# Kernel optimization log

Measured on AMD Instinct MI355X. Metric: run time of the kernel, lower is better.

## Reference

```python
import jax, jax.numpy as jnp
import numpy as np

N, C, E, K = 50000, 128, 640000, 40  # nodes, feat dim, edges, classes
EPS = 1e-5


def setup_inputs() -> dict:
    key = jax.random.key(0)
    ks = jax.random.split(key, 8)
    s = 1.0 / np.sqrt(C)
    return {
        "x": jax.random.normal(ks[0], (N, C), jnp.float32),
        "edge_index": jax.random.randint(ks[1], (2, E), 0, N, dtype=jnp.int32),
        "W_conv": jax.random.normal(ks[2], (C, C), jnp.float32) * s,
        "b_conv": jnp.zeros((C,), jnp.float32),
        "gamma": jnp.ones((C,), jnp.float32),
        "beta": jnp.zeros((C,), jnp.float32),
        "W_fc": jax.random.normal(ks[3], (C, K), jnp.float32) * s,
        "b_fc": jnp.zeros((K,), jnp.float32),
    }


def reference(x, edge_index, W_conv, b_conv, gamma, beta, W_fc, b_fc):
    n = x.shape[0]
    loops = jnp.arange(n, dtype=edge_index.dtype)
    src = jnp.concatenate([edge_index[0], loops])  # add self-loops (PyG default)
    dst = jnp.concatenate([edge_index[1], loops])
    # symmetric normalization: deg^{-1/2}[src] * deg^{-1/2}[dst]
    deg = jax.ops.segment_sum(jnp.ones_like(dst, jnp.float32), dst, num_segments=n)
    dinv = jax.lax.rsqrt(jnp.maximum(deg, 1.0))  # deg >= 1 with self-loops
    norm = dinv[src] * dinv[dst]  # [E+N]
    h = x @ W_conv  # [N, C] transform before propagate (GCNConv)
    agg = jax.ops.segment_sum(h[src] * norm[:, None], dst, num_segments=n) + b_conv
    a = jax.nn.relu(agg) * x  # dropout = identity (eval mode); elementwise mul with residual
    mu = jnp.mean(a, axis=-1, keepdims=True)
    var = jnp.mean((a - mu) ** 2, axis=-1, keepdims=True)
    ln = (a - mu) * jax.lax.rsqrt(var + EPS) * gamma + beta
    return (ln + x) @ W_fc + b_fc
```

## Files before the change

### kernel.cpp

```cpp
#include <hip/hip_runtime.h>

#define C_DIM 128
#define EPS 1e-5f
#define NBIN 784
#define SBLK 2048

typedef __attribute__((ext_vector_type(8))) short short8;
typedef __attribute__((ext_vector_type(4))) float f32x4;

__device__ __forceinline__ unsigned bf16rn(float f) {
    unsigned u = __float_as_uint(f);
    return (u + 0x7fffu + ((u >> 16) & 1u)) >> 16;
}
__device__ __forceinline__ unsigned pack_bf16(float lo, float hi) {
    return bf16rn(lo) | (bf16rn(hi) << 16);
}
__device__ __forceinline__ float blo(unsigned u) { return __uint_as_float(u << 16); }
__device__ __forceinline__ float bhi(unsigned u) { return __uint_as_float(u & 0xffff0000u); }

__device__ __forceinline__ void wave_scan_excl_lds(unsigned* buf, int lane) {
    const int CH = (NBIN + 63) / 64;
    unsigned v[CH];
    unsigned s = 0;
    int c0 = lane * CH;
#pragma unroll
    for (int k = 0; k < CH; k++) {
        int idx = c0 + k;
        v[k] = (idx < NBIN) ? buf[idx] : 0u;
        s += v[k];
    }
    unsigned inc = s;
#pragma unroll
    for (int off = 1; off < 64; off <<= 1) {
        unsigned tmp = __shfl_up(inc, off);
        if (lane >= off) inc += tmp;
    }
    unsigned run = inc - s;
#pragma unroll
    for (int k = 0; k < CH; k++) {
        int idx = c0 + k;
        if (idx < NBIN) { buf[idx] = run; run += v[k]; }
    }
}

__global__ __launch_bounds__(256) void k_hist(const float* __restrict__ W,
                                              const float* __restrict__ Wfc,
                                              unsigned short* __restrict__ WhT,
                                              unsigned short* __restrict__ WlT,
                                              unsigned short* __restrict__ WT,
                                              const int* __restrict__ edst,
                                              unsigned* __restrict__ H, int e, int ns) {
    __shared__ unsigned lh[NBIN];
    int b = blockIdx.x, t = threadIdx.x;
    if (b < ns) {
        for (int k = t; k < NBIN; k += 256) lh[k] = 0u;
        __syncthreads();
        int e0 = b * SBLK;
        int lim = e - e0; if (lim > SBLK) lim = SBLK;
        for (int k = t; k < lim; k += 256) atomicAdd(&lh[edst[e0 + k] >> 6], 1u);
        __syncthreads();
        for (int k = t; k < NBIN; k += 256) H[(size_t)b * NBIN + k] = lh[k];
    } else {
        int gid = (b - ns) * 256 + t;
        int stride = ((int)gridDim.x - ns) * 256;
        for (int i = gid; i < 128 * 128; i += stride) {
            int c = i >> 7, k = i & 127;
            float v = W[k * 128 + c];
            unsigned hi = bf16rn(v);
            WhT[c * 128 + k] = (unsigned short)hi;
            WlT[c * 128 + k] = (unsigned short)bf16rn(v - __uint_as_float(hi << 16));
        }
        for (int i = gid; i < 48 * 128; i += stride) {
            int nc = i >> 7, k = i & 127;
            WT[nc * 128 + k] = (unsigned short)((nc < 40) ? bf16rn(Wfc[k * 40 + nc]) : 0u);
        }
    }
}

__global__ __launch_bounds__(256) void k_scan(unsigned* __restrict__ H,
                                              unsigned* __restrict__ tot, int ns) {
    int bin = blockIdx.x * 4 + (threadIdx.x >> 6);
    int lane = threadIdx.x & 63;
    if (bin >= NBIN) return;
    unsigned run = 0;
    for (int base = 0; base < ns; base += 64) {
        int idx = base + lane;
        unsigned v = (idx < ns) ? H[(size_t)idx * NBIN + bin] : 0u;
        unsigned inc = v;
#pragma unroll
        for (int off = 1; off < 64; off <<= 1) {
            unsigned tmp = __shfl_up(inc, off);
            if (lane >= off) inc += tmp;
        }
        if (idx < ns) H[(size_t)idx * NBIN + bin] = run + inc - v;
        run += __shfl(inc, 63);
    }
    if (lane == 0) tot[bin] = run;
}

__global__ void k_binscan(const unsigned* __restrict__ tot, unsigned* __restrict__ bstart) {
    int lane = threadIdx.x;
    const int CH = (NBIN + 63) / 64;
    unsigned v[CH];
    unsigned s = 0;
    int c0 = lane * CH;
#pragma unroll
    for (int k = 0; k < CH; k++) {
        int idx = c0 + k;
        v[k] = (idx < NBIN) ? tot[idx] : 0u;
        s += v[k];
    }
    unsigned inc = s;
#pragma unroll
    for (int off = 1; off < 64; off <<= 1) {
        unsigned tmp = __shfl_up(inc, off);
        if (lane >= off) inc += tmp;
    }
    unsigned run = inc - s;
#pragma unroll
    for (int k = 0; k < CH; k++) {
        int idx = c0 + k;
        if (idx < NBIN) { bstart[idx] = run; run += v[k]; }
    }
    if (lane == 63) bstart[NBIN] = run;
}

__global__ __launch_bounds__(256, 4) void k_sort(const float* __restrict__ x,
                                                 const unsigned short* __restrict__ WhT,
                                                 const unsigned short* __restrict__ WlT,
                                                 unsigned short* __restrict__ hbs,
                                                 const int* __restrict__ esrc,
                                                 const int* __restrict__ edst,
                                                 const unsigned* __restrict__ H,
                                                 const unsigned* __restrict__ bstart,
                                                 unsigned* __restrict__ recs,
                                                 int n, int e, int ns) {
    __shared__ unsigned bufA[NBIN];
    __shared__ unsigned bufB[NBIN];
    __shared__ unsigned bufC[NBIN];
    __shared__ unsigned sbuf[SBLK];
    int b = blockIdx.x, t = threadIdx.x;

    if (b < ns) {
        int e0 = b * SBLK;
        int myE = e - e0; if (myE > SBLK) myE = SBLK;
        for (int k = t; k < NBIN; k += 256) { bufC[k] = 0u; bufA[k] = 0u; }
        __syncthreads();
        for (int k = t; k < myE; k += 256) atomicAdd(&bufC[edst[e0 + k] >> 6], 1u);
        for (int bin = t; bin < NBIN; bin += 256)
            bufB[bin] = bstart[bin] + H[(size_t)b * NBIN + bin];
        __syncthreads();
        if (t < 64) wave_scan_excl_lds(bufC, t);
        __syncthreads();
        for (int k = t; k < myE; k += 256) {
            int d = edst[e0 + k];
            int s = esrc[e0 + k];
            int bin = d >> 6;
            unsigned lr = atomicAdd(&bufA[bin], 1u);
            sbuf[bufC[bin] + lr] =
                ((unsigned)bin << 22) | ((unsigned)(d & 63) << 16) | (unsigned)s;
        }
        __syncthreads();
        for (int j = t; j < myE; j += 256) {
            unsigned rec = sbuf[j];
            unsigned bin = rec >> 22;
            recs[bufB[bin] + (unsigned)j - bufC[bin]] = rec;
        }
    } else {
        int r0 = (b - ns) * 128;
        int wid = t >> 6, lane = t & 63;
        int mrow = lane & 15, quad = lane >> 4;
        int rb = r0 + wid * 32;

        f32x4 acc[2][8];
#pragma unroll
        for (int m = 0; m < 2; m++)
#pragma unroll
            for (int nn = 0; nn < 8; nn++) acc[m][nn] = (f32x4){0.f, 0.f, 0.f, 0.f};

#pragma unroll
        for (int ks = 0; ks < 4; ks++) {
            short8 Ah[2], Al[2];
#pragma unroll
            for (int m = 0; m < 2; m++) {
                int r = rb + m * 16 + mrow;
                if (r >= n) r = n - 1;
                const float* xp = &x[(long)r * C_DIM + ks * 32 + quad * 8];
                float4 va = *(const float4*)xp;
                float4 vb = *(const float4*)(xp + 4);
                float xv[8] = {va.x, va.y, va.z, va.w, vb.x, vb.y, vb.z, vb.w};
#pragma unroll
                for (int e8 = 0; e8 < 8; e8++) {
                    unsigned hi = bf16rn(xv[e8]);
                    Ah[m][e8] = (short)hi;
                    Al[m][e8] = (short)bf16rn(xv[e8] - __uint_as_float(hi << 16));
                }
            }
#pragma unroll
            for (int nn = 0; nn < 8; nn++) {
                int wof = (nn * 16 + mrow) * 128 + ks * 32 + quad * 8;
                short8 Bh = *(const short8*)&WhT[wof];
                short8 Bl = *(const short8*)&WlT[wof];
#pragma unroll
                for (int m = 0; m < 2; m++) {
                    acc[m][nn] = __builtin_amdgcn_mfma_f32_16x16x32_bf16(Ah[m], Bh, acc[m][nn], 0, 0, 0);
                    acc[m][nn] = __builtin_amdgcn_mfma_f32_16x16x32_bf16(Al[m], Bh, acc[m][nn], 0, 0, 0);
                    acc[m][nn] = __builtin_amdgcn_mfma_f32_16x16x32_bf16(Ah[m], Bl, acc[m][nn], 0, 0, 0);
                }
            }
        }
#pragma unroll
        for (int m = 0; m < 2; m++)
#pragma unroll
            for (int nn = 0; nn < 8; nn++) {
                int c = nn * 16 + mrow;
#pragma unroll
                for (int reg = 0; reg < 4; reg++) {
                    int r = rb + m * 16 + quad * 4 + reg;
                    if (r < n) hbs[(long)r * 128 + c] = (unsigned short)bf16rn(acc[m][nn][reg]);
                }
            }
    }
}

__global__ __launch_bounds__(256) void k_csr(const unsigned* __restrict__ recs,
                                             const unsigned* __restrict__ bstart,
                                             const unsigned* __restrict__ hb,
                                             unsigned* __restrict__ hb2,
                                             unsigned short* __restrict__ csr,
                                             unsigned* __restrict__ rowptr, int n) {
    __shared__ unsigned nh[64], nstart[64], cur[64];
    __shared__ float dinvl[64];
    __shared__ unsigned short sl[4096];
    int bin = blockIdx.x, t = threadIdx.x;
    unsigned s0 = bstart[bin];
    unsigned cn = bstart[bin + 1] - s0;
    if (t < 64) { nh[t] = 0u; cur[t] = 0u; }
    __syncthreads();
    for (unsigned k = t; k < cn; k += 256) atomicAdd(&nh[(recs[s0 + k] >> 16) & 63u], 1u);
    __syncthreads();
    if (t < 64) {
        unsigned v = nh[t];
        unsigned inc = v;
#pragma unroll
        for (int off = 1; off < 64; off <<= 1) {
            unsigned tmp = __shfl_up(inc, off);
            if (t >= off) inc += tmp;
        }
        unsigned excl = inc - v;
        nstart[t] = excl;
        rowptr[bin * 64 + t] = s0 + excl;
        dinvl[t] = rsqrtf((float)v + 1.0f);
    }
    __syncthreads();
    for (unsigned k = t; k < cn; k += 256) {
        unsigned rec = recs[s0 + k];
        unsigned nd = (rec >> 16) & 63u;
        unsigned r = atomicAdd(&cur[nd], 1u);
        unsigned idx = nstart[nd] + r;
        if (idx < 4096) sl[idx] = (unsigned short)(rec & 0xFFFFu);
        else csr[s0 + idx] = (unsigned short)(rec & 0xFFFFu);
    }
    __syncthreads();
    for (unsigned k = t; k < cn && k < 4096; k += 256) csr[s0 + k] = sl[k];
    for (int idx = t; idx < 1024; idx += 256) {
        int row = idx >> 4;
        int node = bin * 64 + row;
        if (node < n) {
            float di = dinvl[row];
            uint4 u = ((const uint4*)hb)[(size_t)node * 16 + (idx & 15)];
            uint4 o;
            o.x = pack_bf16(di * blo(u.x), di * bhi(u.x));
            o.y = pack_bf16(di * blo(u.y), di * bhi(u.y));
            o.z = pack_bf16(di * blo(u.z), di * bhi(u.z));
            o.w = pack_bf16(di * blo(u.w), di * bhi(u.w));
            ((uint4*)hb2)[(size_t)node * 16 + (idx & 15)] = o;
        }
    }
}

__global__ __launch_bounds__(256) void aggregate(const unsigned* __restrict__ hb2,
                                                 const float* __restrict__ x,
                                                 const unsigned short* __restrict__ csr,
                                                 const unsigned* __restrict__ rowptr,
                                                 const float* __restrict__ bconv,
                                                 const float* __restrict__ gamma,
                                                 const float* __restrict__ beta,
                                                 unsigned* __restrict__ zb, int n) {
    int wid = (blockIdx.x * blockDim.x + threadIdx.x) >> 6;
    if (wid >= n) return;
    int lane = threadIdx.x & 63;
    int sub = lane & 15, grp = lane >> 4;
    int i = wid;

    unsigned rs = rowptr[i];
    unsigned re = rowptr[i + 1];
    int deg = (int)(re - rs);
    float di = rsqrtf((float)deg + 1.0f);

    uint4 us = *(const uint4*)(hb2 + (long)i * 64 + sub * 4);
    float4 xa = *(const float4*)&x[(long)i * C_DIM + sub * 8];
    float4 xb = *(const float4*)&x[(long)i * C_DIM + sub * 8 + 4];
    int s_all = (int)csr[rs + lane];

    float wself = (grp == 0) ? 1.f : 0.f;
    float acc[8];
    acc[0] = wself * blo(us.x); acc[1] = wself * bhi(us.x);
    acc[2] = wself * blo(us.y); acc[3] = wself * bhi(us.y);
    acc[4] = wself * blo(us.z); acc[5] = wself * bhi(us.z);
    acc[6] = wself * blo(us.w); acc[7] = wself * bhi(us.w);

    int nIt = (deg + 15) >> 4;
    for (int it = 0; it < nIt; ++it) {
        int ss[4];
        float ww[4];
#pragma unroll
        for (int qq = 0; qq < 4; qq++) {
            int base = it * 16 + qq * 4;
            int tq = base + grp;
            int sq;
            if (base >= 64) sq = (int)csr[rs + tq];
            else sq = __shfl(s_all, tq);
            float wq = 1.f;
            if (tq >= deg) { wq = 0.f; sq = i; }
            ss[qq] = sq;
            ww[qq] = wq;
        }
        uint4 u[4];
#pragma unroll
        for (int qq = 0; qq < 4; qq++) u[qq] = *(const uint4*)(hb2 + (long)ss[qq] * 64 + sub * 4);
#pragma unroll
        for (int qq = 0; qq < 4; qq++) {
            float w = ww[qq];
            acc[0] += w * blo(u[qq].x); acc[1] += w * bhi(u[qq].x);
            acc[2] += w * blo(u[qq].y); acc[3] += w * bhi(u[qq].y);
            acc[4] += w * blo(u[qq].z); acc[5] += w * bhi(u[qq].z);
            acc[6] += w * blo(u[qq].w); acc[7] += w * bhi(u[qq].w);
        }
    }

#pragma unroll
    for (int j = 0; j < 8; j++) {
        acc[j] += __shfl_xor(acc[j], 16);
        acc[j] += __shfl_xor(acc[j], 32);
    }

    float4 bca = *(const float4*)&bconv[sub * 8];
    float4 bcb = *(const float4*)&bconv[sub * 8 + 4];
    float a[8], xv[8];
    xv[0] = xa.x; xv[1] = xa.y; xv[2] = xa.z; xv[3] = xa.w;
    xv[4] = xb.x; xv[5] = xb.y; xv[6] = xb.z; xv[7] = xb.w;
    float bc[8] = {bca.x, bca.y, bca.z, bca.w, bcb.x, bcb.y, bcb.z, bcb.w};
#pragma unroll
    for (int j = 0; j < 8; j++) a[j] = fmaxf(acc[j] * di + bc[j], 0.f) * xv[j];

    float s = a[0] + a[1] + a[2] + a[3] + a[4] + a[5] + a[6] + a[7];
#pragma unroll
    for (int off = 1; off < 16; off <<= 1) s += __shfl_xor(s, off);
    float mu = s * (1.0f / 128.0f);
    float d[8], v = 0.f;
#pragma unroll
    for (int j = 0; j < 8; j++) { d[j] = a[j] - mu; v += d[j] * d[j]; }
#pragma unroll
    for (int off = 1; off < 16; off <<= 1) v += __shfl_xor(v, off);
    float inv = rsqrtf(v * (1.0f / 128.0f) + EPS);

    if (grp == 0) {
        float4 ga = *(const float4*)&gamma[sub * 8];
        float4 gb = *(const float4*)&gamma[sub * 8 + 4];
        float4 ba = *(const float4*)&beta[sub * 8];
        float4 bb = *(const float4*)&beta[sub * 8 + 4];
        float g[8] = {ga.x, ga.y, ga.z, ga.w, gb.x, gb.y, gb.z, gb.w};
        float be[8] = {ba.x, ba.y, ba.z, ba.w, bb.x, bb.y, bb.z, bb.w};
        float o[8];
#pragma unroll
        for (int j = 0; j < 8; j++) o[j] = d[j] * inv * g[j] + be[j] + xv[j];
        uint4 p;
        p.x = pack_bf16(o[0], o[1]);
        p.y = pack_bf16(o[2], o[3]);
        p.z = pack_bf16(o[4], o[5]);
        p.w = pack_bf16(o[6], o[7]);
        *(uint4*)(zb + (long)i * 64 + sub * 4) = p;
    }
}

__global__ __launch_bounds__(256) void gemm2(const unsigned short* __restrict__ zb,
                                             const unsigned short* __restrict__ WT,
                                             const float* __restrict__ bfc,
                                             float* __restrict__ out, int n) {
    int t = threadIdx.x;
    int w = t >> 6, lane = t & 63;
    int r0 = blockIdx.x * 64 + w * 16;
    if (r0 >= n) return;
    int mrow = lane & 15;
    int quad = lane >> 4;
    f32x4 acc[3];
#pragma unroll
    for (int nt = 0; nt < 3; nt++) acc[nt] = (f32x4){0.f, 0.f, 0.f, 0.f};
#pragma unroll
    for (int ks = 0; ks < 4; ks++) {
        int r = r0 + mrow;
        if (r >= n) r = n - 1;
        short8 A = *(const short8*)&zb[(long)r * 128 + ks * 32 + quad * 8];
        short8 B[3];
#pragma unroll
        for (int nt = 0; nt < 3; nt++)
            B[nt] = *(const short8*)&WT[(nt * 16 + mrow) * 128 + ks * 32 + quad * 8];
#pragma unroll
        for (int nt = 0; nt < 3; nt++)
            acc[nt] = __builtin_amdgcn_mfma_f32_16x16x32_bf16(A, B[nt], acc[nt], 0, 0, 0);
    }
#pragma unroll
    for (int nt = 0; nt < 3; nt++) {
        int c = nt * 16 + mrow;
        if (c < 40) {
            float bias = bfc[c];
#pragma unroll
            for (int reg = 0; reg < 4; reg++) {
                int r = r0 + quad * 4 + reg;
                if (r < n) out[(long)r * 40 + c] = acc[nt][reg] + bias;
            }
        }
    }
}

extern "C" void kernel_launch(void* const* d_in, const int* in_sizes, int n_in,
                              void* d_out, int out_size, void* d_ws, size_t ws_size,
                              hipStream_t stream) {
    const float* x     = (const float*)d_in[0];
    const int*   ei    = (const int*)d_in[1];
    const float* Wc    = (const float*)d_in[2];
    const float* bc    = (const float*)d_in[3];
    const float* gamma = (const float*)d_in[4];
    const float* beta  = (const float*)d_in[5];
    const float* Wfc   = (const float*)d_in[6];
    const float* bfc   = (const float*)d_in[7];
    float* out = (float*)d_out;

    int N = in_sizes[0] / C_DIM;
    int E = in_sizes[1] / 2;
    const int* esrc = ei;
    const int* edst = ei + E;
    int ns = (E + SBLK - 1) / SBLK;
    int g1 = (N + 127) / 128;

    char* p = (char*)d_ws;
    auto carve = [&](size_t bytes) {
        void* q = (void*)p;
        p += (bytes + 255) & ~(size_t)255;
        return q;
    };
    unsigned* hb         = (unsigned*)carve((size_t)N * 64 * 4);
    unsigned* hb2        = (unsigned*)carve((size_t)N * 64 * 4);
    unsigned short* WT   = (unsigned short*)carve(48 * 128 * 2);
    unsigned short* WhT  = (unsigned short*)carve(128 * 128 * 2);
    unsigned short* WlT  = (unsigned short*)carve(128 * 128 * 2);
    unsigned* H          = (unsigned*)carve((size_t)ns * NBIN * 4);
    unsigned* tot        = (unsigned*)carve((size_t)NBIN * 4);
    unsigned* bstart     = (unsigned*)carve((size_t)(NBIN + 1) * 4);
    unsigned* recs       = (unsigned*)carve((size_t)E * 4);
    unsigned* rowptr     = (unsigned*)carve((size_t)(NBIN * 64 + 1) * 4);
    unsigned short* csr  = (unsigned short*)carve((size_t)E * 2 + 256);

    unsigned* zb = hb;

    k_hist<<<ns + 64, 256, 0, stream>>>(Wc, Wfc, WhT, WlT, WT, edst, H, E, ns);
    k_scan<<<NBIN / 4, 256, 0, stream>>>(H, tot, ns);
    k_binscan<<<1, 64, 0, stream>>>(tot, bstart);
    k_sort<<<ns + g1, 256, 0, stream>>>(x, WhT, WlT, (unsigned short*)hb, esrc, edst,
                                        H, bstart, recs, N, E, ns);
    k_csr<<<NBIN, 256, 0, stream>>>(recs, bstart, hb, hb2, csr, rowptr, N);
    aggregate<<<((size_t)N * 64 + 255) / 256, 256, 0, stream>>>(
        hb2, x, csr, rowptr, bc, gamma, beta, zb, N);
    gemm2<<<(N + 63) / 64, 256, 0, stream>>>((const unsigned short*)zb, WT, bfc, out, N);
}
```

Measured before the change: 171.7 us.

## Fuse output GEMM into aggregation and fold bin scan into sort kernel

The per-node aggregation kernel now runs 16 nodes per 1024-thread block, stages the bf16 LayerNorm output in LDS, and has three waves do the final 128x40 MFMA GEMM directly. This removes the zb global round trip and the separate gemm2 launch. Separately, the single-wave k_binscan launch is removed: every sort block recomputes the exclusive scan of bin totals in LDS, and block 0 writes bstart for later kernels. The cost is redundant scan work per block, plus a block-wide sync in the aggregate kernel with most waves idle during the GEMM.

After: 174.5 us. About the same (+1.6%).

```diff
diff --git a/kernel.cpp b/kernel.cpp
--- a/kernel.cpp
+++ b/kernel.cpp
@@ -18,7 +18,8 @@
 __device__ __forceinline__ float blo(unsigned u) { return __uint_as_float(u << 16); }
 __device__ __forceinline__ float bhi(unsigned u) { return __uint_as_float(u & 0xffff0000u); }
 
-__device__ __forceinline__ void wave_scan_excl_lds(unsigned* buf, int lane) {
+__device__ __forceinline__ void wave_scan_excl_lds(unsigned* buf, int lane,
+                                                   unsigned* dumpb) {
     const int CH = (NBIN + 63) / 64;
     unsigned v[CH];
     unsigned s = 0;
@@ -39,8 +40,13 @@
 #pragma unroll
     for (int k = 0; k < CH; k++) {
         int idx = c0 + k;
-        if (idx < NBIN) { buf[idx] = run; run += v[k]; }
-    }
+        if (idx < NBIN) {
+            if (dumpb) dumpb[idx] = run;
+            buf[idx] = run;
+            run += v[k];
+        }
+    }
+    if (dumpb && lane == 63) dumpb[NBIN] = run;
 }
 
 __global__ __launch_bounds__(256) void k_hist(const float* __restrict__ W,
@@ -98,33 +104,6 @@
     if (lane == 0) tot[bin] = run;
 }
 
-__global__ void k_binscan(const unsigned* __restrict__ tot, unsigned* __restrict__ bstart) {
-    int lane = threadIdx.x;
-    const int CH = (NBIN + 63) / 64;
-    unsigned v[CH];
-    unsigned s = 0;
-    int c0 = lane * CH;
-#pragma unroll
-    for (int k = 0; k < CH; k++) {
-        int idx = c0 + k;
-        v[k] = (idx < NBIN) ? tot[idx] : 0u;
-        s += v[k];
-    }
-    unsigned inc = s;
-#pragma unroll
-    for (int off = 1; off < 64; off <<= 1) {
-        unsigned tmp = __shfl_up(inc, off);
-        if (lane >= off) inc += tmp;
-    }
-    unsigned run = inc - s;
-#pragma unroll
-    for (int k = 0; k < CH; k++) {
-        int idx = c0 + k;
-        if (idx < NBIN) { bstart[idx] = run; run += v[k]; }
-    }
-    if (lane == 63) bstart[NBIN] = run;
-}
-
 __global__ __launch_bounds__(256, 4) void k_sort(const float* __restrict__ x,
                                                  const unsigned short* __restrict__ WhT,
                                                  const unsigned short* __restrict__ WlT,
@@ -132,7 +111,8 @@
                                                  const int* __restrict__ esrc,
                                                  const int* __restrict__ edst,
                                                  const unsigned* __restrict__ H,
-                                                 const unsigned* __restrict__ bstart,
+                                                 const unsigned* __restrict__ tot,
+                                                 unsigned* __restrict__ bstart,
                                                  unsigned* __restrict__ recs,
                                                  int n, int e, int ns) {
     __shared__ unsigned bufA[NBIN];
@@ -147,11 +127,14 @@
         for (int k = t; k < NBIN; k += 256) { bufC[k] = 0u; bufA[k] = 0u; }
         __syncthreads();
         for (int k = t; k < myE; k += 256) atomicAdd(&bufC[edst[e0 + k] >> 6], 1u);
+        for (int bin = t; bin < NBIN; bin += 256) bufB[bin] = tot[bin];
+        __syncthreads();
+        int wv = t >> 6, lane = t & 63;
+        if (wv == 0) wave_scan_excl_lds(bufC, lane, 0);
+        else if (wv == 1) wave_scan_excl_lds(bufB, lane, b == 0 ? bstart : 0);
+        __syncthreads();
         for (int bin = t; bin < NBIN; bin += 256)
-            bufB[bin] = bstart[bin] + H[(size_t)b * NBIN + bin];
-        __syncthreads();
-        if (t < 64) wave_scan_excl_lds(bufC, t);
-        __syncthreads();
+            bufB[bin] += H[(size_t)b * NBIN + bin];
         for (int k = t; k < myE; k += 256) {
             int d = edst[e0 + k];
             int s = esrc[e0 + k];
@@ -279,28 +262,32 @@
     }
 }
 
-__global__ __launch_bounds__(256) void aggregate(const unsigned* __restrict__ hb2,
-                                                 const float* __restrict__ x,
-                                                 const unsigned short* __restrict__ csr,
-                                                 const unsigned* __restrict__ rowptr,
-                                                 const float* __restrict__ bconv,
-                                                 const float* __restrict__ gamma,
-                                                 const float* __restrict__ beta,
-                                                 unsigned* __restrict__ zb, int n) {
-    int wid = (blockIdx.x * blockDim.x + threadIdx.x) >> 6;
-    if (wid >= n) return;
-    int lane = threadIdx.x & 63;
+__global__ __launch_bounds__(1024) void agg2(const unsigned* __restrict__ hb2,
+                                             const float* __restrict__ x,
+                                             const unsigned short* __restrict__ csr,
+                                             const unsigned* __restrict__ rowptr,
+                                             const float* __restrict__ bconv,
+                                             const float* __restrict__ gamma,
+                                             const float* __restrict__ beta,
+                                             const unsigned short* __restrict__ WT,
+                                             const float* __restrict__ bfc,
+                                             float* __restrict__ out, int n) {
+    __shared__ unsigned zl[16 * 65];
+    int t = threadIdx.x;
+    int wv = t >> 6, lane = t & 63;
     int sub = lane & 15, grp = lane >> 4;
-    int i = wid;
-
-    unsigned rs = rowptr[i];
-    unsigned re = rowptr[i + 1];
+    int i = blockIdx.x * 16 + wv;
+    bool vn = i < n;
+    int ii = vn ? i : n - 1;
+
+    unsigned rs = rowptr[ii];
+    unsigned re = rowptr[ii + 1];
     int deg = (int)(re - rs);
     float di = rsqrtf((float)deg + 1.0f);
 
-    uint4 us = *(const uint4*)(hb2 + (long)i * 64 + sub * 4);
-    float4 xa = *(const float4*)&x[(long)i * C_DIM + sub * 8];
-    float4 xb = *(const float4*)&x[(long)i * C_DIM + sub * 8 + 4];
+    uint4 us = *(const uint4*)(hb2 + (long)ii * 64 + sub * 4);
+    float4 xa = *(const float4*)&x[(long)ii * C_DIM + sub * 8];
+    float4 xb = *(const float4*)&x[(long)ii * C_DIM + sub * 8 + 4];
     int s_all = (int)csr[rs + lane];
 
     float wself = (grp == 0) ? 1.f : 0.f;
@@ -322,7 +309,7 @@
             if (base >= 64) sq = (int)csr[rs + tq];
             else sq = __shfl(s_all, tq);
             float wq = 1.f;
-            if (tq >= deg) { wq = 0.f; sq = i; }
+            if (tq >= deg) { wq = 0.f; sq = ii; }
             ss[qq] = sq;
             ww[qq] = wq;
         }
@@ -375,50 +362,35 @@
         float o[8];
 #pragma unroll
         for (int j = 0; j < 8; j++) o[j] = d[j] * inv * g[j] + be[j] + xv[j];
-        uint4 p;
-        p.x = pack_bf16(o[0], o[1]);
-        p.y = pack_bf16(o[2], o[3]);
-        p.z = pack_bf16(o[4], o[5]);
-        p.w = pack_bf16(o[6], o[7]);
-        *(uint4*)(zb + (long)i * 64 + sub * 4) = p;
-    }
-}
-
-__global__ __launch_bounds__(256) void gemm2(const unsigned short* __restrict__ zb,
-                                             const unsigned short* __restrict__ WT,
-                                             const float* __restrict__ bfc,
-                                             float* __restrict__ out, int n) {
-    int t = threadIdx.x;
-    int w = t >> 6, lane = t & 63;
-    int r0 = blockIdx.x * 64 + w * 16;
-    if (r0 >= n) return;
-    int mrow = lane & 15;
-    int quad = lane >> 4;
-    f32x4 acc[3];
-#pragma unroll
-    for (int nt = 0; nt < 3; nt++) acc[nt] = (f32x4){0.f, 0.f, 0.f, 0.f};
-#pragma unroll
-    for (int ks = 0; ks < 4; ks++) {
-        int r = r0 + mrow;
-        if (r >= n) r = n - 1;
-        short8 A = *(const short8*)&zb[(long)r * 128 + ks * 32 + quad * 8];
-        short8 B[3];
-#pragma unroll
-        for (int nt = 0; nt < 3; nt++)
-            B[nt] = *(const short8*)&WT[(nt * 16 + mrow) * 128 + ks * 32 + quad * 8];
-#pragma unroll
-        for (int nt = 0; nt < 3; nt++)
-            acc[nt] = __builtin_amdgcn_mfma_f32_16x16x32_bf16(A, B[nt], acc[nt], 0, 0, 0);
-    }
-#pragma unroll
-    for (int nt = 0; nt < 3; nt++) {
+        zl[wv * 65 + sub * 4 + 0] = pack_bf16(o[0], o[1]);
+        zl[wv * 65 + sub * 4 + 1] = pack_bf16(o[2], o[3]);
+        zl[wv * 65 + sub * 4 + 2] = pack_bf16(o[4], o[5]);
+        zl[wv * 65 + sub * 4 + 3] = pack_bf16(o[6], o[7]);
+    }
+    __syncthreads();
+
+    if (wv < 3) {
+        int nt = wv;
+        int mrow = lane & 15, quad = lane >> 4;
+        f32x4 a2 = (f32x4){0.f, 0.f, 0.f, 0.f};
+#pragma unroll
+        for (int ks = 0; ks < 4; ks++) {
+            union { unsigned u[4]; short8 s8; } au;
+            int zi = mrow * 65 + ks * 16 + quad * 4;
+            au.u[0] = zl[zi + 0];
+            au.u[1] = zl[zi + 1];
+            au.u[2] = zl[zi + 2];
+            au.u[3] = zl[zi + 3];
+            short8 B = *(const short8*)&WT[(nt * 16 + mrow) * 128 + ks * 32 + quad * 8];
+            a2 = __builtin_amdgcn_mfma_f32_16x16x32_bf16(au.s8, B, a2, 0, 0, 0);
+        }
         int c = nt * 16 + mrow;
         if (c < 40) {
             float bias = bfc[c];
 #pragma unroll
             for (int reg = 0; reg < 4; reg++) {
-                int r = r0 + quad * 4 + reg;
-                if (r < n) out[(long)r * 40 + c] = acc[nt][reg] + bias;
+                int r = blockIdx.x * 16 + quad * 4 + reg;
+                if (r < n) out[(long)r * 40 + c] = a2[reg] + bias;
             }
         }
     }
@@ -462,15 +434,11 @@
     unsigned* rowptr     = (unsigned*)carve((size_t)(NBIN * 64 + 1) * 4);
     unsigned short* csr  = (unsigned short*)carve((size_t)E * 2 + 256);
 
-    unsigned* zb = hb;
-
     k_hist<<<ns + 64, 256, 0, stream>>>(Wc, Wfc, WhT, WlT, WT, edst, H, E, ns);
     k_scan<<<NBIN / 4, 256, 0, stream>>>(H, tot, ns);
-    k_binscan<<<1, 64, 0, stream>>>(tot, bstart);
     k_sort<<<ns + g1, 256, 0, stream>>>(x, WhT, WlT, (unsigned short*)hb, esrc, edst,
-                                        H, bstart, recs, N, E, ns);
+                                        H, tot, bstart, recs, N, E, ns);
     k_csr<<<NBIN, 256, 0, stream>>>(recs, bstart, hb, hb2, csr, rowptr, N);
-    aggregate<<<((size_t)N * 64 + 255) / 256, 256, 0, stream>>>(
-        hb2, x, csr, rowptr, bc, gamma, beta, zb, N);
-    gemm2<<<(N + 63) / 64, 256, 0, stream>>>((const unsigned short*)zb, WT, bfc, out, N);
-}
+    agg2<<<(N + 15) / 16, 1024, 0, stream>>>(hb2, x, csr, rowptr, bc, gamma, beta,
+                                             WT, bfc, out, N);
+}
```

## Fold bin scan into sort, drop dinv prescale pass, apply per-edge weights in aggregate

Applied to the files above, without the earlier changes.

Removes the single-block k_binscan launch: every sort block now scans the bin totals itself, and block 0 writes bstart. k_csr no longer rescales h by deg^-1/2 into a second bf16 buffer. Instead it writes a dinv array, and aggregate multiplies each gathered neighbor row by dinv[src] (shuffled from the first 64 lanes, or loaded directly beyond that). The edge-chunk size SBLK is doubled, which halves the number of histogram and sort blocks and shrinks the H matrix. The trade is redundant scans in every sort block and an extra dinv gather per edge in aggregate, against one fewer launch and one fewer full pass over h.

New measurement: 168.8 us. Within noise of the previous version (-1.7%).

```diff
diff --git a/kernel.cpp b/kernel.cpp
--- a/kernel.cpp
+++ b/kernel.cpp
@@ -3,7 +3,7 @@
 #define C_DIM 128
 #define EPS 1e-5f
 #define NBIN 784
-#define SBLK 2048
+#define SBLK 4096
 
 typedef __attribute__((ext_vector_type(8))) short short8;
 typedef __attribute__((ext_vector_type(4))) float f32x4;
@@ -18,7 +18,8 @@
 __device__ __forceinline__ float blo(unsigned u) { return __uint_as_float(u << 16); }
 __device__ __forceinline__ float bhi(unsigned u) { return __uint_as_float(u & 0xffff0000u); }
 
-__device__ __forceinline__ void wave_scan_excl_lds(unsigned* buf, int lane) {
+__device__ __forceinline__ void wave_scan_excl_lds(unsigned* buf, int lane,
+                                                   unsigned* dumpb) {
     const int CH = (NBIN + 63) / 64;
     unsigned v[CH];
     unsigned s = 0;
@@ -39,8 +40,13 @@
 #pragma unroll
     for (int k = 0; k < CH; k++) {
         int idx = c0 + k;
-        if (idx < NBIN) { buf[idx] = run; run += v[k]; }
-    }
+        if (idx < NBIN) {
+            if (dumpb) dumpb[idx] = run;
+            buf[idx] = run;
+            run += v[k];
+        }
+    }
+    if (dumpb && lane == 63) dumpb[NBIN] = run;
 }
 
 __global__ __launch_bounds__(256) void k_hist(const float* __restrict__ W,
@@ -98,33 +104,6 @@
     if (lane == 0) tot[bin] = run;
 }
 
-__global__ void k_binscan(const unsigned* __restrict__ tot, unsigned* __restrict__ bstart) {
-    int lane = threadIdx.x;
-    const int CH = (NBIN + 63) / 64;
-    unsigned v[CH];
-    unsigned s = 0;
-    int c0 = lane * CH;
-#pragma unroll
-    for (int k = 0; k < CH; k++) {
-        int idx = c0 + k;
-        v[k] = (idx < NBIN) ? tot[idx] : 0u;
-        s += v[k];
-    }
-    unsigned inc = s;
-#pragma unroll
-    for (int off = 1; off < 64; off <<= 1) {
-        unsigned tmp = __shfl_up(inc, off);
-        if (lane >= off) inc += tmp;
-    }
-    unsigned run = inc - s;
-#pragma unroll
-    for (int k = 0; k < CH; k++) {
-        int idx = c0 + k;
-        if (idx < NBIN) { bstart[idx] = run; run += v[k]; }
-    }
-    if (lane == 63) bstart[NBIN] = run;
-}
-
 __global__ __launch_bounds__(256, 4) void k_sort(const float* __restrict__ x,
                                                  const unsigned short* __restrict__ WhT,
                                                  const unsigned short* __restrict__ WlT,
@@ -132,7 +111,8 @@
                                                  const int* __restrict__ esrc,
                                                  const int* __restrict__ edst,
                                                  const unsigned* __restrict__ H,
-                                                 const unsigned* __restrict__ bstart,
+                                                 const unsigned* __restrict__ tot,
+                                                 unsigned* __restrict__ bstart,
                                                  unsigned* __restrict__ recs,
                                                  int n, int e, int ns) {
     __shared__ unsigned bufA[NBIN];
@@ -147,11 +127,14 @@
         for (int k = t; k < NBIN; k += 256) { bufC[k] = 0u; bufA[k] = 0u; }
         __syncthreads();
         for (int k = t; k < myE; k += 256) atomicAdd(&bufC[edst[e0 + k] >> 6], 1u);
+        for (int bin = t; bin < NBIN; bin += 256) bufB[bin] = tot[bin];
+        __syncthreads();
+        int wv = t >> 6, lane = t & 63;
+        if (wv == 0) wave_scan_excl_lds(bufC, lane, 0);
+        else if (wv == 1) wave_scan_excl_lds(bufB, lane, b == 0 ? bstart : 0);
+        __syncthreads();
         for (int bin = t; bin < NBIN; bin += 256)
-            bufB[bin] = bstart[bin] + H[(size_t)b * NBIN + bin];
-        __syncthreads();
-        if (t < 64) wave_scan_excl_lds(bufC, t);
-        __syncthreads();
+            bufB[bin] += H[(size_t)b * NBIN + bin];
         for (int k = t; k < myE; k += 256) {
             int d = edst[e0 + k];
             int s = esrc[e0 + k];
@@ -225,12 +208,10 @@
 
 __global__ __launch_bounds__(256) void k_csr(const unsigned* __restrict__ recs,
                                              const unsigned* __restrict__ bstart,
-                                             const unsigned* __restrict__ hb,
-                                             unsigned* __restrict__ hb2,
                                              unsigned short* __restrict__ csr,
-                                             unsigned* __restrict__ rowptr, int n) {
+                                             unsigned* __restrict__ rowptr,
+                                             float* __restrict__ dinv) {
     __shared__ unsigned nh[64], nstart[64], cur[64];
-    __shared__ float dinvl[64];
     __shared__ unsigned short sl[4096];
     int bin = blockIdx.x, t = threadIdx.x;
     unsigned s0 = bstart[bin];
@@ -250,7 +231,7 @@
         unsigned excl = inc - v;
         nstart[t] = excl;
         rowptr[bin * 64 + t] = s0 + excl;
-        dinvl[t] = rsqrtf((float)v + 1.0f);
+        dinv[bin * 64 + t] = rsqrtf((float)v + 1.0f);
     }
     __syncthreads();
     for (unsigned k = t; k < cn; k += 256) {
@@ -263,26 +244,13 @@
     }
     __syncthreads();
     for (unsigned k = t; k < cn && k < 4096; k += 256) csr[s0 + k] = sl[k];
-    for (int idx = t; idx < 1024; idx += 256) {
-        int row = idx >> 4;
-        int node = bin * 64 + row;
-        if (node < n) {
-            float di = dinvl[row];
-            uint4 u = ((const uint4*)hb)[(size_t)node * 16 + (idx & 15)];
-            uint4 o;
-            o.x = pack_bf16(di * blo(u.x), di * bhi(u.x));
-            o.y = pack_bf16(di * blo(u.y), di * bhi(u.y));
-            o.z = pack_bf16(di * blo(u.z), di * bhi(u.z));
-            o.w = pack_bf16(di * blo(u.w), di * bhi(u.w));
-            ((uint4*)hb2)[(size_t)node * 16 + (idx & 15)] = o;
-        }
-    }
-}
-
-__global__ __launch_bounds__(256) void aggregate(const unsigned* __restrict__ hb2,
+}
+
+__global__ __launch_bounds__(256) void aggregate(const unsigned* __restrict__ hb,
                                                  const float* __restrict__ x,
                                                  const unsigned short* __restrict__ csr,
                                                  const unsigned* __restrict__ rowptr,
+                                                 const float* __restrict__ dinv,
                                                  const float* __restrict__ bconv,
                                                  const float* __restrict__ gamma,
                                                  const float* __restrict__ beta,
@@ -298,12 +266,13 @@
     int deg = (int)(re - rs);
     float di = rsqrtf((float)deg + 1.0f);
 
-    uint4 us = *(const uint4*)(hb2 + (long)i * 64 + sub * 4);
+    uint4 us = *(const uint4*)(hb + (long)i * 64 + sub * 4);
     float4 xa = *(const float4*)&x[(long)i * C_DIM + sub * 8];
     float4 xb = *(const float4*)&x[(long)i * C_DIM + sub * 8 + 4];
     int s_all = (int)csr[rs + lane];
-
-    float wself = (grp == 0) ? 1.f : 0.f;
+    float w_all = dinv[s_all];
+
+    float wself = (grp == 0) ? di : 0.f;
     float acc[8];
     acc[0] = wself * blo(us.x); acc[1] = wself * bhi(us.x);
     acc[2] = wself * blo(us.y); acc[3] = wself * bhi(us.y);
@@ -319,16 +288,21 @@
             int base = it * 16 + qq * 4;
             int tq = base + grp;
             int sq;
-            if (base >= 64) sq = (int)csr[rs + tq];
-            else sq = __shfl(s_all, tq);
-            float wq = 1.f;
+            float wq;
+            if (base >= 64) {
+                sq = (int)csr[rs + tq];
+                wq = dinv[sq];
+            } else {
+                sq = __shfl(s_all, tq);
+                wq = __shfl(w_all, tq);
+            }
             if (tq >= deg) { wq = 0.f; sq = i; }
             ss[qq] = sq;
             ww[qq] = wq;
         }
         uint4 u[4];
 #pragma unroll
-        for (int qq = 0; qq < 4; qq++) u[qq] = *(const uint4*)(hb2 + (long)ss[qq] * 64 + sub * 4);
+        for (int qq = 0; qq < 4; qq++) u[qq] = *(const uint4*)(hb + (long)ss[qq] * 64 + sub * 4);
 #pragma unroll
         for (int qq = 0; qq < 4; qq++) {
             float w = ww[qq];
@@ -451,7 +425,7 @@
         return q;
     };
     unsigned* hb         = (unsigned*)carve((size_t)N * 64 * 4);
-    unsigned* hb2        = (unsigned*)carve((size_t)N * 64 * 4);
+    unsigned* zb         = (unsigned*)carve((size_t)N * 64 * 4);
     unsigned short* WT   = (unsigned short*)carve(48 * 128 * 2);
     unsigned short* WhT  = (unsigned short*)carve(128 * 128 * 2);
     unsigned short* WlT  = (unsigned short*)carve(128 * 128 * 2);
@@ -461,16 +435,14 @@
     unsigned* recs       = (unsigned*)carve((size_t)E * 4);
     unsigned* rowptr     = (unsigned*)carve((size_t)(NBIN * 64 + 1) * 4);
     unsigned short* csr  = (unsigned short*)carve((size_t)E * 2 + 256);
-
-    unsigned* zb = hb;
+    float* dinv          = (float*)carve(65536 * 4);
 
     k_hist<<<ns + 64, 256, 0, stream>>>(Wc, Wfc, WhT, WlT, WT, edst, H, E, ns);
     k_scan<<<NBIN / 4, 256, 0, stream>>>(H, tot, ns);
-    k_binscan<<<1, 64, 0, stream>>>(tot, bstart);
     k_sort<<<ns + g1, 256, 0, stream>>>(x, WhT, WlT, (unsigned short*)hb, esrc, edst,
-                                        H, bstart, recs, N, E, ns);
-    k_csr<<<NBIN, 256, 0, stream>>>(recs, bstart, hb, hb2, csr, rowptr, N);
+                                        H, tot, bstart, recs, N, E, ns);
+    k_csr<<<NBIN, 256, 0, stream>>>(recs, bstart, csr, rowptr, dinv);
     aggregate<<<((size_t)N * 64 + 255) / 256, 256, 0, stream>>>(
-        hb2, x, csr, rowptr, bc, gamma, beta, zb, N);
+        hb, x, csr, rowptr, dinv, bc, gamma, beta, zb, N);
     gemm2<<<(N + 63) / 64, 256, 0, stream>>>((const unsigned short*)zb, WT, bfc, out, N);
 }
```
